# Kernel tuning notes

Measured on AMD Instinct MI355X. Metric: run time of the kernel, lower is better.

## Reference

```python
import jax, jax.numpy as jnp
import numpy as np

SEQ_LEN = 512
DIM = 256
HEADS = 8
DIM_HEAD = 32
INNER = HEADS * DIM_HEAD
BATCH = 1
LN_EPS = 1e-5


def setup_inputs() -> dict:
    key = jax.random.key(0)
    ks = jax.random.split(key, 6)
    # kaiming_uniform_(a=sqrt(5)) on [L, in, out] -> bound = 1/sqrt(fan_in) with fan_in = in_dim*out_dim? 
    # torch computes fan_in from dims [1:] => fan_in = in_dim (dim of -2) * ... in practice bound ~ sqrt(1/fan_in);
    # exact init distribution is irrelevant for correctness testing, use uniform(+-1/sqrt(DIM)).
    s = 1.0 / np.sqrt(DIM)
    so = 1.0 / np.sqrt(INNER)
    return {
        "x": jax.random.normal(ks[0], (BATCH, SEQ_LEN, DIM), jnp.float32),
        "Wq": jax.random.uniform(ks[1], (SEQ_LEN, DIM, INNER), jnp.float32, -s, s),
        "Wk": jax.random.uniform(ks[2], (SEQ_LEN, DIM, INNER), jnp.float32, -s, s),
        "Wv": jax.random.uniform(ks[3], (SEQ_LEN, DIM, INNER), jnp.float32, -s, s),
        "gamma": jnp.ones((DIM,), jnp.float32),
        "beta": jnp.zeros((DIM,), jnp.float32),
        "Wo": jax.random.uniform(ks[4], (INNER, DIM), jnp.float32, -so, so),
        "bo": jnp.zeros((DIM,), jnp.float32),
    }


def reference(x, Wq, Wk, Wv, gamma, beta, Wo, bo):
    b, n, dim = x.shape
    h, dh = HEADS, DIM_HEAD
    # LayerNorm
    mu = jnp.mean(x, axis=-1, keepdims=True)
    var = jnp.mean((x - mu) ** 2, axis=-1, keepdims=True)
    xn = (x - mu) / jnp.sqrt(var + LN_EPS) * gamma + beta
    # Per-relative-index projections: pd[b, r, m, e] = xn[b, m] @ W[r]
    qd = jnp.einsum('bmc,rce->brme', xn, Wq)
    kd = jnp.einsum('bmc,rce->brme', xn, Wk)
    vd = jnp.einsum('bmc,rce->brme', xn, Wv)
    i = jnp.arange(n)
    # to_q / to_v index map: max(0, i - j); to_k (after rearrange swap) uses min(0, m - n) + n - 1
    rq = jnp.maximum(0, i[:, None] - i[None, :])          # [n(query), m(key)]
    rk = jnp.minimum(0, i[None, :] - i[:, None]) + n - 1  # [n, m]
    # q[b,n,m,e] = qd[b, rq[n,m], m]; k[b,n,m,e] = kd[b, rk[n,m], n]; v like q
    q_full = qd[:, rq, i[None, :], :].reshape(b, n, n, h, dh)
    k_full = kd[:, rk, i[:, None], :].reshape(b, n, n, h, dh)
    v_full = vd[:, rq, i[None, :], :].reshape(b, n, n, h, dh)
    scale = dh ** -0.5
    dots = jnp.einsum('bnmhd,bnmhd->bhnm', q_full, k_full) * scale
    causal = i[:, None] >= i[None, :]  # tril
    dots = jnp.where(causal[None, None], dots, -jnp.inf)
    attn = jax.nn.softmax(dots, axis=-1)
    out = jnp.einsum('bhnm,bnmhd->bnhd', attn, v_full).reshape(b, n, h * dh)
    return out @ Wo + bo
```

## Files before the change

### kernel.cpp

```cpp
#include <hip/hip_runtime.h>
#include <hip/hip_bf16.h>

typedef unsigned short u16;
typedef unsigned int   u32;
typedef __bf16 bf16x8 __attribute__((ext_vector_type(8)));
typedef float  f32x4  __attribute__((ext_vector_type(4)));
typedef u32    u32x4  __attribute__((ext_vector_type(4)));
typedef u32    u32x2  __attribute__((ext_vector_type(2)));

#define TRI_TOTAL 131328

__device__ __forceinline__ float b2f(u16 u) {
    return __builtin_bit_cast(float, ((u32)u) << 16);
}
__device__ __forceinline__ u16 f2b(float f) {
    u32 u = __builtin_bit_cast(u32, f);
    return (u16)((u + 0x7fffu + ((u >> 16) & 1u)) >> 16);
}
__device__ __forceinline__ int pcol(int col) {
    return (((col & 7) ^ ((col >> 3) & 7)) << 4);
}

__global__ void __launch_bounds__(256) ln_kernel(const float* __restrict__ x,
                                                 const float* __restrict__ g,
                                                 const float* __restrict__ b,
                                                 u16* __restrict__ xn) {
    int n = blockIdx.x, t = threadIdx.x;
    float v = x[n * 256 + t];
    __shared__ float red[4];
    float s = v;
    #pragma unroll
    for (int o = 32; o >= 1; o >>= 1) s += __shfl_xor(s, o);
    if ((t & 63) == 0) red[t >> 6] = s;
    __syncthreads();
    float mu = (red[0] + red[1] + red[2] + red[3]) * (1.0f / 256.0f);
    float d = v - mu;
    __syncthreads();
    float s2 = d * d;
    #pragma unroll
    for (int o = 32; o >= 1; o >>= 1) s2 += __shfl_xor(s2, o);
    if ((t & 63) == 0) red[t >> 6] = s2;
    __syncthreads();
    float var = (red[0] + red[1] + red[2] + red[3]) * (1.0f / 256.0f);
    float y = d * rsqrtf(var + 1e-5f) * g[t] + b[t];
    xn[n * 256 + t] = f2b(y);
}

__global__ void __launch_bounds__(256) proj_kernel(
        const u16* __restrict__ xn,
        const float* __restrict__ Wq, const float* __restrict__ Wk,
        const float* __restrict__ Wv,
        u16* __restrict__ Qa, u16* __restrict__ Ka, u16* __restrict__ Va) {
    __shared__ u16 Wl[64 * 256];
    __shared__ u16 Al[64 * 256];

    int bid = blockIdx.x;
    int which = bid >> 11;
    int rr = bid & 2047;
    int r  = (which == 1) ? (511 - (rr >> 2)) : (rr >> 2);
    int cs = rr & 3;
    const float* W = (which == 0) ? Wq : ((which == 1) ? Wk : Wv);
    u16* Out       = (which == 0) ? Qa : ((which == 1) ? Ka : Va);
    int rows  = (which == 1) ? (r + 1) : (512 - r);
    int pbase = (which == 1) ? (511 - r) : 0;
    int nbase = (which == 1) ? (511 - r) : r;

    int t = threadIdx.x;
    int c0 = cs * 64;

    int srow   = t >> 5;
    int slot16 = (t & 31) * 16;
    char* adp = (char*)Al + srow * 512 + (slot16 ^ (srow << 4));
    u32x4 ar0, ar1, ar2, ar3, ar4, ar5, ar6, ar7;

#define A_LOAD(M0) do {                                                       \
    int gg;                                                                   \
    gg = pbase + (M0) +  0 + srow; if (gg > 511) gg = 511;                    \
    ar0 = *(const u32x4*)((const char*)xn + (size_t)gg * 512 + slot16);       \
    gg = pbase + (M0) +  8 + srow; if (gg > 511) gg = 511;                    \
    ar1 = *(const u32x4*)((const char*)xn + (size_t)gg * 512 + slot16);       \
    gg = pbase + (M0) + 16 + srow; if (gg > 511) gg = 511;                    \
    ar2 = *(const u32x4*)((const char*)xn + (size_t)gg * 512 + slot16);       \
    gg = pbase + (M0) + 24 + srow; if (gg > 511) gg = 511;                    \
    ar3 = *(const u32x4*)((const char*)xn + (size_t)gg * 512 + slot16);       \
    gg = pbase + (M0) + 32 + srow; if (gg > 511) gg = 511;                    \
    ar4 = *(const u32x4*)((const char*)xn + (size_t)gg * 512 + slot16);       \
    gg = pbase + (M0) + 40 + srow; if (gg > 511) gg = 511;                    \
    ar5 = *(const u32x4*)((const char*)xn + (size_t)gg * 512 + slot16);       \
    gg = pbase + (M0) + 48 + srow; if (gg > 511) gg = 511;                    \
    ar6 = *(const u32x4*)((const char*)xn + (size_t)gg * 512 + slot16);       \
    gg = pbase + (M0) + 56 + srow; if (gg > 511) gg = 511;                    \
    ar7 = *(const u32x4*)((const char*)xn + (size_t)gg * 512 + slot16);       \
} while (0)

#define A_WRITE() do {                                                        \
    *(u32x4*)(adp + 0 * 4096) = ar0;                                          \
    *(u32x4*)(adp + 1 * 4096) = ar1;                                          \
    *(u32x4*)(adp + 2 * 4096) = ar2;                                          \
    *(u32x4*)(adp + 3 * 4096) = ar3;                                          \
    *(u32x4*)(adp + 4 * 4096) = ar4;                                          \
    *(u32x4*)(adp + 5 * 4096) = ar5;                                          \
    *(u32x4*)(adp + 6 * 4096) = ar6;                                          \
    *(u32x4*)(adp + 7 * 4096) = ar7;                                          \
} while (0)

    {
        int c4 = (t & 15) * 4;
        int kq = t >> 4;
        const float* wp = W + ((size_t)r << 16) + c0 + c4 + (size_t)(kq * 4) * 256;
        f32x4 w00 = *(const f32x4*)(wp + 0);
        f32x4 w01 = *(const f32x4*)(wp + 256);
        f32x4 w02 = *(const f32x4*)(wp + 512);
        f32x4 w03 = *(const f32x4*)(wp + 768);
        f32x4 w10 = *(const f32x4*)(wp + 16384 + 0);
        f32x4 w11 = *(const f32x4*)(wp + 16384 + 256);
        f32x4 w12 = *(const f32x4*)(wp + 16384 + 512);
        f32x4 w13 = *(const f32x4*)(wp + 16384 + 768);
        f32x4 w20 = *(const f32x4*)(wp + 32768 + 0);
        f32x4 w21 = *(const f32x4*)(wp + 32768 + 256);
        f32x4 w22 = *(const f32x4*)(wp + 32768 + 512);
        f32x4 w23 = *(const f32x4*)(wp + 32768 + 768);
        f32x4 w30 = *(const f32x4*)(wp + 49152 + 0);
        f32x4 w31 = *(const f32x4*)(wp + 49152 + 256);
        f32x4 w32 = *(const f32x4*)(wp + 49152 + 512);
        f32x4 w33 = *(const f32x4*)(wp + 49152 + 768);
        A_LOAD(0);
#define WLW(IT, VA, VB, VC, VD) {                                             \
        int kbase2 = (kq * 4 + (IT) * 64) * 2;                                \
        _Pragma("unroll")                                                     \
        for (int i = 0; i < 4; ++i) {                                         \
            int col = c4 + i;                                                 \
            u32 lo = (u32)f2b(VA[i]) | ((u32)f2b(VB[i]) << 16);               \
            u32 hi = (u32)f2b(VC[i]) | ((u32)f2b(VD[i]) << 16);               \
            u32x2 pr; pr[0] = lo; pr[1] = hi;                                 \
            *(u32x2*)((char*)Wl + col * 512 + (kbase2 ^ pcol(col))) = pr;     \
        }                                                                     \
    }
        WLW(0, w00, w01, w02, w03)
        WLW(1, w10, w11, w12, w13)
        WLW(2, w20, w21, w22, w23)
        WLW(3, w30, w31, w32, w33)
#undef WLW
    }

    int wv  = t >> 6;
    int rg  = wv >> 1;
    int cg  = wv & 1;
    int L   = t & 63;
    int l15 = L & 15, l4 = L >> 4;
    const char* wb = (const char*)Wl;
    const char* a_base = (const char*)Al + (rg * 32 + l15) * 512;
    int am = (l15 & 7) << 4;
    int cA = cg * 32 + l15, cB = cA + 16;
    int swA = pcol(cA), swB = pcol(cB);

    for (int m0 = 0; m0 < rows; m0 += 64) {
        A_WRITE();
        __syncthreads();
        if (m0 + 64 < rows) A_LOAD(m0 + 64);

        f32x4 acc00 = {}, acc01 = {}, acc10 = {}, acc11 = {};
#define KS(ks) {                                                              \
        int kb = (ks) * 64 + l4 * 16;                                         \
        bf16x8 a0 = *(const bf16x8*)(a_base + (kb ^ am));                     \
        bf16x8 a1 = *(const bf16x8*)(a_base + 16 * 512 + (kb ^ am));          \
        bf16x8 b0 = *(const bf16x8*)(wb + cA * 512 + (kb ^ swA));             \
        bf16x8 b1 = *(const bf16x8*)(wb + cB * 512 + (kb ^ swB));             \
        acc00 = __builtin_amdgcn_mfma_f32_16x16x32_bf16(a0, b0, acc00, 0, 0, 0); \
        acc01 = __builtin_amdgcn_mfma_f32_16x16x32_bf16(a0, b1, acc01, 0, 0, 0); \
        acc10 = __builtin_amdgcn_mfma_f32_16x16x32_bf16(a1, b0, acc10, 0, 0, 0); \
        acc11 = __builtin_amdgcn_mfma_f32_16x16x32_bf16(a1, b1, acc11, 0, 0, 0); \
    }
        KS(0) KS(1) KS(2) KS(3) KS(4) KS(5) KS(6) KS(7)
#undef KS

        #pragma unroll
        for (int rf = 0; rf < 2; ++rf) {
            #pragma unroll
            for (int j = 0; j < 4; ++j) {
                int ml = m0 + rg * 32 + rf * 16 + l4 * 4 + j;
                if (ml < rows) {
                    int nout = nbase + ml;
                    size_t prow = (size_t)(nout * (nout + 1) / 2) + (size_t)ml;
                    u16* op = Out + prow * 256 + c0 + cg * 32 + l15;
                    f32x4 va = rf ? acc10 : acc00;
                    f32x4 vb = rf ? acc11 : acc01;
                    op[0]  = f2b(va[j]);
                    op[16] = f2b(vb[j]);
                }
            }
        }
        __syncthreads();
    }
#undef A_LOAD
#undef A_WRITE
}

__global__ void __launch_bounds__(256) attn_kernel(const u16* __restrict__ Qa,
                                                   const u16* __restrict__ Ka,
                                                   const u16* __restrict__ Va,
                                                   float* __restrict__ ao) {
    int n = blockIdx.x, t = threadIdx.x;
    __shared__ float pbuf[512 * 9];
    __shared__ float linv[8];
    int band = n + 1;
    size_t rb = (size_t)(n * (n + 1) / 2);

    int h = t & 7, mi = t >> 3;
    for (int m0 = 0; m0 < band; m0 += 32) {
        int m = m0 + mi;
        float d = -1e30f;
        if (m < band) {
            const char* qp = (const char*)Qa + (rb + m) * 512 + h * 64;
            const char* kp = (const char*)Ka + (rb + m) * 512 + h * 64;
            float acc = 0.f;
            #pragma unroll
            for (int cch = 0; cch < 4; ++cch) {
                u32x4 qv = *reinterpret_cast<const u32x4*>(qp + cch * 16);
                u32x4 kv = *reinterpret_cast<const u32x4*>(kp + cch * 16);
                #pragma unroll
                for (int i = 0; i < 4; ++i) {
                    float ql = __builtin_bit_cast(float, qv[i] << 16);
                    float qh = __builtin_bit_cast(float, qv[i] & 0xffff0000u);
                    float kl = __builtin_bit_cast(float, kv[i] << 16);
                    float kh = __builtin_bit_cast(float, kv[i] & 0xffff0000u);
                    acc += ql * kl + qh * kh;
                }
            }
            d = acc * 0.17677669529663687f;
        }
        pbuf[m * 9 + h] = d;
    }
    __syncthreads();

    int wv = t >> 6, L = t & 63;
    for (int s = 0; s < 2; ++s) {
        int hh = wv + s * 4;
        float mx = -1e30f;
        for (int m = L; m < band; m += 64) mx = fmaxf(mx, pbuf[m * 9 + hh]);
        #pragma unroll
        for (int o = 32; o >= 1; o >>= 1) mx = fmaxf(mx, __shfl_xor(mx, o));
        float sum = 0.f;
        for (int m = L; m < band; m += 64) {
            float p = __expf(pbuf[m * 9 + hh] - mx);
            pbuf[m * 9 + hh] = p;
            sum += p;
        }
        #pragma unroll
        for (int o = 32; o >= 1; o >>= 1) sum += __shfl_xor(sum, o);
        if (L == 0) linv[hh] = 1.0f / sum;
    }
    __syncthreads();

    int h2 = t >> 5;
    const char* vp = (const char*)Va + rb * 512 + (size_t)t * 2;
    const float* pb = pbuf + h2;
    float a0 = 0, a1 = 0, a2 = 0, a3 = 0;
    int m = 0;
    for (; m + 4 <= band; m += 4) {
        a0 += pb[(m + 0) * 9] * b2f(*(const u16*)(vp + (size_t)(m + 0) * 512));
        a1 += pb[(m + 1) * 9] * b2f(*(const u16*)(vp + (size_t)(m + 1) * 512));
        a2 += pb[(m + 2) * 9] * b2f(*(const u16*)(vp + (size_t)(m + 2) * 512));
        a3 += pb[(m + 3) * 9] * b2f(*(const u16*)(vp + (size_t)(m + 3) * 512));
    }
    for (; m < band; ++m)
        a0 += pb[m * 9] * b2f(*(const u16*)(vp + (size_t)m * 512));
    ao[n * 256 + t] = ((a0 + a1) + (a2 + a3)) * linv[h2];
}

__global__ void __launch_bounds__(256) outproj_kernel(const float* __restrict__ ao,
                                                      const float* __restrict__ Wo,
                                                      const float* __restrict__ bo,
                                                      float* __restrict__ out) {
    int n = blockIdx.x, e = threadIdx.x;
    const float* a = ao + n * 256;
    float c0 = bo[e], c1 = 0, c2 = 0, c3 = 0;
    for (int c = 0; c < 256; c += 4) {
        c0 += a[c + 0] * Wo[(c + 0) * 256 + e];
        c1 += a[c + 1] * Wo[(c + 1) * 256 + e];
        c2 += a[c + 2] * Wo[(c + 2) * 256 + e];
        c3 += a[c + 3] * Wo[(c + 3) * 256 + e];
    }
    out[n * 256 + e] = (c0 + c1) + (c2 + c3);
}

extern "C" void kernel_launch(void* const* d_in, const int* in_sizes, int n_in,
                              void* d_out, int out_size, void* d_ws, size_t ws_size,
                              hipStream_t stream) {
    const float* x     = (const float*)d_in[0];
    const float* Wq    = (const float*)d_in[1];
    const float* Wk    = (const float*)d_in[2];
    const float* Wv    = (const float*)d_in[3];
    const float* gamma = (const float*)d_in[4];
    const float* beta  = (const float*)d_in[5];
    const float* Wo    = (const float*)d_in[6];
    const float* bo    = (const float*)d_in[7];
    float* out = (float*)d_out;

    char* ws = (char*)d_ws;
    u16* xn = (u16*)ws;
    size_t off = (size_t)512 * 256 * 2;
    u16* Qa = (u16*)(ws + off); off += (size_t)TRI_TOTAL * 256 * 2;
    u16* Ka = (u16*)(ws + off); off += (size_t)TRI_TOTAL * 256 * 2;
    u16* Va = (u16*)(ws + off); off += (size_t)TRI_TOTAL * 256 * 2;
    float* ao = (float*)(ws + off);

    ln_kernel<<<512, 256, 0, stream>>>(x, gamma, beta, xn);
    proj_kernel<<<6144, 256, 0, stream>>>(xn, Wq, Wk, Wv, Qa, Ka, Va);
    attn_kernel<<<512, 256, 0, stream>>>(Qa, Ka, Va, ao);
    outproj_kernel<<<512, 256, 0, stream>>>(ao, Wo, bo, out);
}
```

Measured before the change: 275.1 us.

## Process two relative-index weight slices per projection block with prefetched second weights

```diff
diff --git a/kernel.cpp b/kernel.cpp
--- a/kernel.cpp
+++ b/kernel.cpp
@@ -46,7 +46,7 @@
     xn[n * 256 + t] = f2b(y);
 }
 
-__global__ void __launch_bounds__(256) proj_kernel(
+__global__ void __launch_bounds__(256, 2) proj_kernel(
         const u16* __restrict__ xn,
         const float* __restrict__ Wq, const float* __restrict__ Wk,
         const float* __restrict__ Wv,
@@ -55,15 +55,20 @@
     __shared__ u16 Al[64 * 256];
 
     int bid = blockIdx.x;
-    int which = bid >> 11;
-    int rr = bid & 2047;
-    int r  = (which == 1) ? (511 - (rr >> 2)) : (rr >> 2);
+    int which = bid >> 10;
+    int rr = bid & 1023;
+    int g  = rr >> 2;
     int cs = rr & 3;
     const float* W = (which == 0) ? Wq : ((which == 1) ? Wk : Wv);
     u16* Out       = (which == 0) ? Qa : ((which == 1) ? Ka : Va);
-    int rows  = (which == 1) ? (r + 1) : (512 - r);
-    int pbase = (which == 1) ? (511 - r) : 0;
-    int nbase = (which == 1) ? (511 - r) : r;
+    int rA = (which == 1) ? (511 - 2 * g) : (2 * g);
+    int rB = (which == 1) ? (510 - 2 * g) : (2 * g + 1);
+    int rows0 = (which == 1) ? (rA + 1) : (512 - rA);
+    int pb0   = (which == 1) ? (511 - rA) : 0;
+    int nb0   = (which == 1) ? (511 - rA) : rA;
+    int rows1 = (which == 1) ? (rB + 1) : (512 - rB);
+    int pb1   = (which == 1) ? (511 - rB) : 0;
+    int nb1   = (which == 1) ? (511 - rB) : rB;
 
     int t = threadIdx.x;
     int c0 = cs * 64;
@@ -73,23 +78,23 @@
     char* adp = (char*)Al + srow * 512 + (slot16 ^ (srow << 4));
     u32x4 ar0, ar1, ar2, ar3, ar4, ar5, ar6, ar7;
 
-#define A_LOAD(M0) do {                                                       \
+#define A_LOAD(PB, M0) do {                                                   \
     int gg;                                                                   \
-    gg = pbase + (M0) +  0 + srow; if (gg > 511) gg = 511;                    \
+    gg = (PB) + (M0) +  0 + srow; if (gg > 511) gg = 511;                     \
     ar0 = *(const u32x4*)((const char*)xn + (size_t)gg * 512 + slot16);       \
-    gg = pbase + (M0) +  8 + srow; if (gg > 511) gg = 511;                    \
+    gg = (PB) + (M0) +  8 + srow; if (gg > 511) gg = 511;                     \
     ar1 = *(const u32x4*)((const char*)xn + (size_t)gg * 512 + slot16);       \
-    gg = pbase + (M0) + 16 + srow; if (gg > 511) gg = 511;                    \
+    gg = (PB) + (M0) + 16 + srow; if (gg > 511) gg = 511;                     \
     ar2 = *(const u32x4*)((const char*)xn + (size_t)gg * 512 + slot16);       \
-    gg = pbase + (M0) + 24 + srow; if (gg > 511) gg = 511;                    \
+    gg = (PB) + (M0) + 24 + srow; if (gg > 511) gg = 511;                     \
     ar3 = *(const u32x4*)((const char*)xn + (size_t)gg * 512 + slot16);       \
-    gg = pbase + (M0) + 32 + srow; if (gg > 511) gg = 511;                    \
+    gg = (PB) + (M0) + 32 + srow; if (gg > 511) gg = 511;                     \
     ar4 = *(const u32x4*)((const char*)xn + (size_t)gg * 512 + slot16);       \
-    gg = pbase + (M0) + 40 + srow; if (gg > 511) gg = 511;                    \
+    gg = (PB) + (M0) + 40 + srow; if (gg > 511) gg = 511;                     \
     ar5 = *(const u32x4*)((const char*)xn + (size_t)gg * 512 + slot16);       \
-    gg = pbase + (M0) + 48 + srow; if (gg > 511) gg = 511;                    \
+    gg = (PB) + (M0) + 48 + srow; if (gg > 511) gg = 511;                     \
     ar6 = *(const u32x4*)((const char*)xn + (size_t)gg * 512 + slot16);       \
-    gg = pbase + (M0) + 56 + srow; if (gg > 511) gg = 511;                    \
+    gg = (PB) + (M0) + 56 + srow; if (gg > 511) gg = 511;                     \
     ar7 = *(const u32x4*)((const char*)xn + (size_t)gg * 512 + slot16);       \
 } while (0)
 
@@ -104,27 +109,27 @@
     *(u32x4*)(adp + 7 * 4096) = ar7;                                          \
 } while (0)
 
-    {
-        int c4 = (t & 15) * 4;
-        int kq = t >> 4;
-        const float* wp = W + ((size_t)r << 16) + c0 + c4 + (size_t)(kq * 4) * 256;
-        f32x4 w00 = *(const f32x4*)(wp + 0);
-        f32x4 w01 = *(const f32x4*)(wp + 256);
-        f32x4 w02 = *(const f32x4*)(wp + 512);
-        f32x4 w03 = *(const f32x4*)(wp + 768);
-        f32x4 w10 = *(const f32x4*)(wp + 16384 + 0);
-        f32x4 w11 = *(const f32x4*)(wp + 16384 + 256);
-        f32x4 w12 = *(const f32x4*)(wp + 16384 + 512);
-        f32x4 w13 = *(const f32x4*)(wp + 16384 + 768);
-        f32x4 w20 = *(const f32x4*)(wp + 32768 + 0);
-        f32x4 w21 = *(const f32x4*)(wp + 32768 + 256);
-        f32x4 w22 = *(const f32x4*)(wp + 32768 + 512);
-        f32x4 w23 = *(const f32x4*)(wp + 32768 + 768);
-        f32x4 w30 = *(const f32x4*)(wp + 49152 + 0);
-        f32x4 w31 = *(const f32x4*)(wp + 49152 + 256);
-        f32x4 w32 = *(const f32x4*)(wp + 49152 + 512);
-        f32x4 w33 = *(const f32x4*)(wp + 49152 + 768);
-        A_LOAD(0);
+    int c4 = (t & 15) * 4;
+    int kq = t >> 4;
+    f32x4 w00, w01, w02, w03, w10, w11, w12, w13;
+    f32x4 w20, w21, w22, w23, w30, w31, w32, w33;
+
+#define W_LOAD(R) do {                                                        \
+    const float* wp = W + ((size_t)(R) << 16) + c0 + c4 + (size_t)(kq * 4) * 256; \
+    w00 = *(const f32x4*)(wp + 0);           w01 = *(const f32x4*)(wp + 256); \
+    w02 = *(const f32x4*)(wp + 512);         w03 = *(const f32x4*)(wp + 768); \
+    w10 = *(const f32x4*)(wp + 16384 + 0);   w11 = *(const f32x4*)(wp + 16384 + 256); \
+    w12 = *(const f32x4*)(wp + 16384 + 512); w13 = *(const f32x4*)(wp + 16384 + 768); \
+    w20 = *(const f32x4*)(wp + 32768 + 0);   w21 = *(const f32x4*)(wp + 32768 + 256); \
+    w22 = *(const f32x4*)(wp + 32768 + 512); w23 = *(const f32x4*)(wp + 32768 + 768); \
+    w30 = *(const f32x4*)(wp + 49152 + 0);   w31 = *(const f32x4*)(wp + 49152 + 256); \
+    w32 = *(const f32x4*)(wp + 49152 + 512); w33 = *(const f32x4*)(wp + 49152 + 768); \
+} while (0)
+
+#define W_PIN() asm volatile("" :: "v"(w00), "v"(w01), "v"(w02), "v"(w03),    \
+    "v"(w10), "v"(w11), "v"(w12), "v"(w13), "v"(w20), "v"(w21), "v"(w22),     \
+    "v"(w23), "v"(w30), "v"(w31), "v"(w32), "v"(w33))
+
 #define WLW(IT, VA, VB, VC, VD) {                                             \
         int kbase2 = (kq * 4 + (IT) * 64) * 2;                                \
         _Pragma("unroll")                                                     \
@@ -136,12 +141,12 @@
             *(u32x2*)((char*)Wl + col * 512 + (kbase2 ^ pcol(col))) = pr;     \
         }                                                                     \
     }
-        WLW(0, w00, w01, w02, w03)
-        WLW(1, w10, w11, w12, w13)
-        WLW(2, w20, w21, w22, w23)
-        WLW(3, w30, w31, w32, w33)
-#undef WLW
-    }
+#define WL_WRITE() do {                                                       \
+        WLW(0, w00, w01, w02, w03)                                            \
+        WLW(1, w10, w11, w12, w13)                                            \
+        WLW(2, w20, w21, w22, w23)                                            \
+        WLW(3, w30, w31, w32, w33)                                            \
+} while (0)
 
     int wv  = t >> 6;
     int rg  = wv >> 1;
@@ -154,12 +159,6 @@
     int cA = cg * 32 + l15, cB = cA + 16;
     int swA = pcol(cA), swB = pcol(cB);
 
-    for (int m0 = 0; m0 < rows; m0 += 64) {
-        A_WRITE();
-        __syncthreads();
-        if (m0 + 64 < rows) A_LOAD(m0 + 64);
-
-        f32x4 acc00 = {}, acc01 = {}, acc10 = {}, acc11 = {};
 #define KS(ks) {                                                              \
         int kb = (ks) * 64 + l4 * 16;                                         \
         bf16x8 a0 = *(const bf16x8*)(a_base + (kb ^ am));                     \
@@ -171,29 +170,56 @@
         acc10 = __builtin_amdgcn_mfma_f32_16x16x32_bf16(a1, b0, acc10, 0, 0, 0); \
         acc11 = __builtin_amdgcn_mfma_f32_16x16x32_bf16(a1, b1, acc11, 0, 0, 0); \
     }
-        KS(0) KS(1) KS(2) KS(3) KS(4) KS(5) KS(6) KS(7)
+
+#define MTILE(M0, ROWS, NB, PREF) {                                           \
+        A_WRITE();                                                            \
+        __syncthreads();                                                      \
+        PREF                                                                  \
+        f32x4 acc00 = {}, acc01 = {}, acc10 = {}, acc11 = {};                 \
+        KS(0) KS(1) KS(2) KS(3) KS(4) KS(5) KS(6) KS(7)                       \
+        _Pragma("unroll")                                                     \
+        for (int rf = 0; rf < 2; ++rf) {                                      \
+            _Pragma("unroll")                                                 \
+            for (int j = 0; j < 4; ++j) {                                     \
+                int ml = (M0) + rg * 32 + rf * 16 + l4 * 4 + j;               \
+                if (ml < (ROWS)) {                                            \
+                    int nout = (NB) + ml;                                     \
+                    size_t prow = (size_t)(nout * (nout + 1) / 2) + (size_t)ml; \
+                    u16* op = Out + prow * 256 + c0 + cg * 32 + l15;          \
+                    f32x4 va = rf ? acc10 : acc00;                            \
+                    f32x4 vb = rf ? acc11 : acc01;                            \
+                    op[0]  = f2b(va[j]);                                      \
+                    op[16] = f2b(vb[j]);                                      \
+                }                                                             \
+            }                                                                 \
+        }                                                                     \
+        __syncthreads();                                                      \
+    }
+
+    W_LOAD(rA);
+    A_LOAD(pb0, 0);
+    WL_WRITE();
+    MTILE(0, rows0, nb0,
+          { W_LOAD(rB); W_PIN();
+            if (64 < rows0) { A_LOAD(pb0, 64); } else { A_LOAD(pb1, 0); } })
+    for (int m0 = 64; m0 < rows0; m0 += 64) {
+        MTILE(m0, rows0, nb0,
+              { if (m0 + 64 < rows0) { A_LOAD(pb0, m0 + 64); }
+                else { A_LOAD(pb1, 0); } })
+    }
+    WL_WRITE();
+    for (int m0 = 0; m0 < rows1; m0 += 64) {
+        MTILE(m0, rows1, nb1,
+              { if (m0 + 64 < rows1) { A_LOAD(pb1, m0 + 64); } })
+    }
+#undef MTILE
 #undef KS
-
-        #pragma unroll
-        for (int rf = 0; rf < 2; ++rf) {
-            #pragma unroll
-            for (int j = 0; j < 4; ++j) {
-                int ml = m0 + rg * 32 + rf * 16 + l4 * 4 + j;
-                if (ml < rows) {
-                    int nout = nbase + ml;
-                    size_t prow = (size_t)(nout * (nout + 1) / 2) + (size_t)ml;
-                    u16* op = Out + prow * 256 + c0 + cg * 32 + l15;
-                    f32x4 va = rf ? acc10 : acc00;
-                    f32x4 vb = rf ? acc11 : acc01;
-                    op[0]  = f2b(va[j]);
-                    op[16] = f2b(vb[j]);
-                }
-            }
-        }
-        __syncthreads();
-    }
+#undef WL_WRITE
+#undef WLW
+#undef W_PIN
+#undef W_LOAD
+#undef A_WRITE
 #undef A_LOAD
-#undef A_WRITE
 }
 
 __global__ void __launch_bounds__(256) attn_kernel(const u16* __restrict__ Qa,
@@ -306,7 +332,7 @@
     float* ao = (float*)(ws + off);
 
     ln_kernel<<<512, 256, 0, stream>>>(x, gamma, beta, xn);
-    proj_kernel<<<6144, 256, 0, stream>>>(xn, Wq, Wk, Wv, Qa, Ka, Va);
+    proj_kernel<<<3072, 256, 0, stream>>>(xn, Wq, Wk, Wv, Qa, Ka, Va);
     attn_kernel<<<512, 256, 0, stream>>>(Qa, Ka, Va, ao);
     outproj_kernel<<<512, 256, 0, stream>>>(ao, Wo, bo, out);
 }
```

New measurement: 276.4 us. About the same (+0.4%).

## Keep projection weight fragments in registers instead of shared memory

Applied to the files above, without the earlier changes.

```diff
diff --git a/kernel.cpp b/kernel.cpp
--- a/kernel.cpp
+++ b/kernel.cpp
@@ -6,7 +6,6 @@
 typedef __bf16 bf16x8 __attribute__((ext_vector_type(8)));
 typedef float  f32x4  __attribute__((ext_vector_type(4)));
 typedef u32    u32x4  __attribute__((ext_vector_type(4)));
-typedef u32    u32x2  __attribute__((ext_vector_type(2)));
 
 #define TRI_TOTAL 131328
 
@@ -16,9 +15,6 @@
 __device__ __forceinline__ u16 f2b(float f) {
     u32 u = __builtin_bit_cast(u32, f);
     return (u16)((u + 0x7fffu + ((u >> 16) & 1u)) >> 16);
-}
-__device__ __forceinline__ int pcol(int col) {
-    return (((col & 7) ^ ((col >> 3) & 7)) << 4);
 }
 
 __global__ void __launch_bounds__(256) ln_kernel(const float* __restrict__ x,
@@ -46,12 +42,11 @@
     xn[n * 256 + t] = f2b(y);
 }
 
-__global__ void __launch_bounds__(256) proj_kernel(
+__global__ void __launch_bounds__(256, 2) proj_kernel(
         const u16* __restrict__ xn,
         const float* __restrict__ Wq, const float* __restrict__ Wk,
         const float* __restrict__ Wv,
         u16* __restrict__ Qa, u16* __restrict__ Ka, u16* __restrict__ Va) {
-    __shared__ u16 Wl[64 * 256];
     __shared__ u16 Al[64 * 256];
 
     int bid = blockIdx.x;
@@ -67,6 +62,11 @@
 
     int t = threadIdx.x;
     int c0 = cs * 64;
+    int wv  = t >> 6;
+    int rg  = wv >> 1;
+    int cg  = wv & 1;
+    int L   = t & 63;
+    int l15 = L & 15, l4 = L >> 4;
 
     int srow   = t >> 5;
     int slot16 = (t & 31) * 16;
@@ -104,55 +104,27 @@
     *(u32x4*)(adp + 7 * 4096) = ar7;                                          \
 } while (0)
 
-    {
-        int c4 = (t & 15) * 4;
-        int kq = t >> 4;
-        const float* wp = W + ((size_t)r << 16) + c0 + c4 + (size_t)(kq * 4) * 256;
-        f32x4 w00 = *(const f32x4*)(wp + 0);
-        f32x4 w01 = *(const f32x4*)(wp + 256);
-        f32x4 w02 = *(const f32x4*)(wp + 512);
-        f32x4 w03 = *(const f32x4*)(wp + 768);
-        f32x4 w10 = *(const f32x4*)(wp + 16384 + 0);
-        f32x4 w11 = *(const f32x4*)(wp + 16384 + 256);
-        f32x4 w12 = *(const f32x4*)(wp + 16384 + 512);
-        f32x4 w13 = *(const f32x4*)(wp + 16384 + 768);
-        f32x4 w20 = *(const f32x4*)(wp + 32768 + 0);
-        f32x4 w21 = *(const f32x4*)(wp + 32768 + 256);
-        f32x4 w22 = *(const f32x4*)(wp + 32768 + 512);
-        f32x4 w23 = *(const f32x4*)(wp + 32768 + 768);
-        f32x4 w30 = *(const f32x4*)(wp + 49152 + 0);
-        f32x4 w31 = *(const f32x4*)(wp + 49152 + 256);
-        f32x4 w32 = *(const f32x4*)(wp + 49152 + 512);
-        f32x4 w33 = *(const f32x4*)(wp + 49152 + 768);
-        A_LOAD(0);
-#define WLW(IT, VA, VB, VC, VD) {                                             \
-        int kbase2 = (kq * 4 + (IT) * 64) * 2;                                \
-        _Pragma("unroll")                                                     \
-        for (int i = 0; i < 4; ++i) {                                         \
-            int col = c4 + i;                                                 \
-            u32 lo = (u32)f2b(VA[i]) | ((u32)f2b(VB[i]) << 16);               \
-            u32 hi = (u32)f2b(VC[i]) | ((u32)f2b(VD[i]) << 16);               \
-            u32x2 pr; pr[0] = lo; pr[1] = hi;                                 \
-            *(u32x2*)((char*)Wl + col * 512 + (kbase2 ^ pcol(col))) = pr;     \
-        }                                                                     \
-    }
-        WLW(0, w00, w01, w02, w03)
-        WLW(1, w10, w11, w12, w13)
-        WLW(2, w20, w21, w22, w23)
-        WLW(3, w30, w31, w32, w33)
-#undef WLW
-    }
-
-    int wv  = t >> 6;
-    int rg  = wv >> 1;
-    int cg  = wv & 1;
-    int L   = t & 63;
-    int l15 = L & 15, l4 = L >> 4;
-    const char* wb = (const char*)Wl;
+    A_LOAD(0);
+
+    const float* wbase = W + ((size_t)r << 16) + c0 + cg * 32 + l15;
+    bf16x8 b00, b01, b02, b03, b04, b05, b06, b07;
+    bf16x8 b10, b11, b12, b13, b14, b15, b16, b17;
+#define BLOAD(HF, KSI, DST) {                                                 \
+    const float* wp = wbase + (size_t)((KSI) * 32 + l4 * 8) * 256 + (HF) * 16;\
+    u32x4 pk;                                                                 \
+    pk[0] = (u32)f2b(wp[0])    | ((u32)f2b(wp[256])  << 16);                  \
+    pk[1] = (u32)f2b(wp[512])  | ((u32)f2b(wp[768])  << 16);                  \
+    pk[2] = (u32)f2b(wp[1024]) | ((u32)f2b(wp[1280]) << 16);                  \
+    pk[3] = (u32)f2b(wp[1536]) | ((u32)f2b(wp[1792]) << 16);                  \
+    DST = __builtin_bit_cast(bf16x8, pk); }
+    BLOAD(0, 0, b00) BLOAD(0, 1, b01) BLOAD(0, 2, b02) BLOAD(0, 3, b03)
+    BLOAD(0, 4, b04) BLOAD(0, 5, b05) BLOAD(0, 6, b06) BLOAD(0, 7, b07)
+    BLOAD(1, 0, b10) BLOAD(1, 1, b11) BLOAD(1, 2, b12) BLOAD(1, 3, b13)
+    BLOAD(1, 4, b14) BLOAD(1, 5, b15) BLOAD(1, 6, b16) BLOAD(1, 7, b17)
+#undef BLOAD
+
     const char* a_base = (const char*)Al + (rg * 32 + l15) * 512;
     int am = (l15 & 7) << 4;
-    int cA = cg * 32 + l15, cB = cA + 16;
-    int swA = pcol(cA), swB = pcol(cB);
 
     for (int m0 = 0; m0 < rows; m0 += 64) {
         A_WRITE();
@@ -164,12 +136,10 @@
         int kb = (ks) * 64 + l4 * 16;                                         \
         bf16x8 a0 = *(const bf16x8*)(a_base + (kb ^ am));                     \
         bf16x8 a1 = *(const bf16x8*)(a_base + 16 * 512 + (kb ^ am));          \
-        bf16x8 b0 = *(const bf16x8*)(wb + cA * 512 + (kb ^ swA));             \
-        bf16x8 b1 = *(const bf16x8*)(wb + cB * 512 + (kb ^ swB));             \
-        acc00 = __builtin_amdgcn_mfma_f32_16x16x32_bf16(a0, b0, acc00, 0, 0, 0); \
-        acc01 = __builtin_amdgcn_mfma_f32_16x16x32_bf16(a0, b1, acc01, 0, 0, 0); \
-        acc10 = __builtin_amdgcn_mfma_f32_16x16x32_bf16(a1, b0, acc10, 0, 0, 0); \
-        acc11 = __builtin_amdgcn_mfma_f32_16x16x32_bf16(a1, b1, acc11, 0, 0, 0); \
+        acc00 = __builtin_amdgcn_mfma_f32_16x16x32_bf16(a0, b0##ks, acc00, 0, 0, 0); \
+        acc01 = __builtin_amdgcn_mfma_f32_16x16x32_bf16(a0, b1##ks, acc01, 0, 0, 0); \
+        acc10 = __builtin_amdgcn_mfma_f32_16x16x32_bf16(a1, b0##ks, acc10, 0, 0, 0); \
+        acc11 = __builtin_amdgcn_mfma_f32_16x16x32_bf16(a1, b1##ks, acc11, 0, 0, 0); \
     }
         KS(0) KS(1) KS(2) KS(3) KS(4) KS(5) KS(6) KS(7)
 #undef KS
@@ -192,8 +162,8 @@
         }
         __syncthreads();
     }
+#undef A_WRITE
 #undef A_LOAD
-#undef A_WRITE
 }
 
 __global__ void __launch_bounds__(256) attn_kernel(const u16* __restrict__ Qa,
```

Measured after the change: 312.7 us. 1.14x slower.

## Double-buffer projection A tiles via direct global-to-LDS loads, keep W in registers

Applied to the files above, without the earlier changes.

```diff
diff --git a/kernel.cpp b/kernel.cpp
--- a/kernel.cpp
+++ b/kernel.cpp
@@ -19,6 +19,11 @@
 }
 __device__ __forceinline__ int pcol(int col) {
     return (((col & 7) ^ ((col >> 3) & 7)) << 4);
+}
+__device__ __forceinline__ void gload_lds16(const void* g, void* l) {
+    __builtin_amdgcn_global_load_lds(
+        (const __attribute__((address_space(1))) void*)g,
+        (__attribute__((address_space(3))) void*)l, 16, 0, 0);
 }
 
 __global__ void __launch_bounds__(256) ln_kernel(const float* __restrict__ x,
@@ -51,8 +56,9 @@
         const float* __restrict__ Wq, const float* __restrict__ Wk,
         const float* __restrict__ Wv,
         u16* __restrict__ Qa, u16* __restrict__ Ka, u16* __restrict__ Va) {
-    __shared__ u16 Wl[64 * 256];
-    __shared__ u16 Al[64 * 256];
+    __shared__ char lds[65536];
+    char* buf0 = lds;
+    char* buf1 = lds + 32768;
 
     int bid = blockIdx.x;
     int which = bid >> 11;
@@ -67,42 +73,25 @@
 
     int t = threadIdx.x;
     int c0 = cs * 64;
-
-    int srow   = t >> 5;
-    int slot16 = (t & 31) * 16;
-    char* adp = (char*)Al + srow * 512 + (slot16 ^ (srow << 4));
-    u32x4 ar0, ar1, ar2, ar3, ar4, ar5, ar6, ar7;
-
-#define A_LOAD(M0) do {                                                       \
-    int gg;                                                                   \
-    gg = pbase + (M0) +  0 + srow; if (gg > 511) gg = 511;                    \
-    ar0 = *(const u32x4*)((const char*)xn + (size_t)gg * 512 + slot16);       \
-    gg = pbase + (M0) +  8 + srow; if (gg > 511) gg = 511;                    \
-    ar1 = *(const u32x4*)((const char*)xn + (size_t)gg * 512 + slot16);       \
-    gg = pbase + (M0) + 16 + srow; if (gg > 511) gg = 511;                    \
-    ar2 = *(const u32x4*)((const char*)xn + (size_t)gg * 512 + slot16);       \
-    gg = pbase + (M0) + 24 + srow; if (gg > 511) gg = 511;                    \
-    ar3 = *(const u32x4*)((const char*)xn + (size_t)gg * 512 + slot16);       \
-    gg = pbase + (M0) + 32 + srow; if (gg > 511) gg = 511;                    \
-    ar4 = *(const u32x4*)((const char*)xn + (size_t)gg * 512 + slot16);       \
-    gg = pbase + (M0) + 40 + srow; if (gg > 511) gg = 511;                    \
-    ar5 = *(const u32x4*)((const char*)xn + (size_t)gg * 512 + slot16);       \
-    gg = pbase + (M0) + 48 + srow; if (gg > 511) gg = 511;                    \
-    ar6 = *(const u32x4*)((const char*)xn + (size_t)gg * 512 + slot16);       \
-    gg = pbase + (M0) + 56 + srow; if (gg > 511) gg = 511;                    \
-    ar7 = *(const u32x4*)((const char*)xn + (size_t)gg * 512 + slot16);       \
+    int wv  = t >> 6;
+    int rg  = wv >> 1;
+    int cg  = wv & 1;
+    int L   = t & 63;
+    int l15 = L & 15, l4 = L >> 4;
+
+#define DMA_TILE(DST, M0) do {                                                \
+    _Pragma("unroll")                                                         \
+    for (int j = 0; j < 8; ++j) {                                             \
+        int lrow = wv * 16 + 2 * j + (L >> 5);                                \
+        int grow = pbase + (M0) + lrow; if (grow > 511) grow = 511;           \
+        const char* gp = (const char*)xn + (size_t)grow * 512                 \
+                         + (((L & 31) ^ (lrow & 7)) << 4);                    \
+        char* lp = (DST) + (wv * 16 + 2 * j) * 512;                           \
+        gload_lds16(gp, lp);                                                  \
+    }                                                                         \
 } while (0)
 
-#define A_WRITE() do {                                                        \
-    *(u32x4*)(adp + 0 * 4096) = ar0;                                          \
-    *(u32x4*)(adp + 1 * 4096) = ar1;                                          \
-    *(u32x4*)(adp + 2 * 4096) = ar2;                                          \
-    *(u32x4*)(adp + 3 * 4096) = ar3;                                          \
-    *(u32x4*)(adp + 4 * 4096) = ar4;                                          \
-    *(u32x4*)(adp + 5 * 4096) = ar5;                                          \
-    *(u32x4*)(adp + 6 * 4096) = ar6;                                          \
-    *(u32x4*)(adp + 7 * 4096) = ar7;                                          \
-} while (0)
+    DMA_TILE(buf1, 0);
 
     {
         int c4 = (t & 15) * 4;
@@ -124,7 +113,6 @@
         f32x4 w31 = *(const f32x4*)(wp + 49152 + 256);
         f32x4 w32 = *(const f32x4*)(wp + 49152 + 512);
         f32x4 w33 = *(const f32x4*)(wp + 49152 + 768);
-        A_LOAD(0);
 #define WLW(IT, VA, VB, VC, VD) {                                             \
         int kbase2 = (kq * 4 + (IT) * 64) * 2;                                \
         _Pragma("unroll")                                                     \
@@ -133,7 +121,7 @@
             u32 lo = (u32)f2b(VA[i]) | ((u32)f2b(VB[i]) << 16);               \
             u32 hi = (u32)f2b(VC[i]) | ((u32)f2b(VD[i]) << 16);               \
             u32x2 pr; pr[0] = lo; pr[1] = hi;                                 \
-            *(u32x2*)((char*)Wl + col * 512 + (kbase2 ^ pcol(col))) = pr;     \
+            *(u32x2*)(buf0 + col * 512 + (kbase2 ^ pcol(col))) = pr;          \
         }                                                                     \
     }
         WLW(0, w00, w01, w02, w03)
@@ -142,34 +130,40 @@
         WLW(3, w30, w31, w32, w33)
 #undef WLW
     }
-
-    int wv  = t >> 6;
-    int rg  = wv >> 1;
-    int cg  = wv & 1;
-    int L   = t & 63;
-    int l15 = L & 15, l4 = L >> 4;
-    const char* wb = (const char*)Wl;
-    const char* a_base = (const char*)Al + (rg * 32 + l15) * 512;
+    __syncthreads();
+
+    bf16x8 b00, b01, b02, b03, b04, b05, b06, b07;
+    bf16x8 b10, b11, b12, b13, b14, b15, b16, b17;
+#define BEXT(HF, KSI, DST) {                                                  \
+    int col = cg * 32 + (HF) * 16 + l15;                                      \
+    int kb = (KSI) * 64 + l4 * 16;                                            \
+    DST = *(const bf16x8*)(buf0 + col * 512 + (kb ^ pcol(col))); }
+    BEXT(0, 0, b00) BEXT(0, 1, b01) BEXT(0, 2, b02) BEXT(0, 3, b03)
+    BEXT(0, 4, b04) BEXT(0, 5, b05) BEXT(0, 6, b06) BEXT(0, 7, b07)
+    BEXT(1, 0, b10) BEXT(1, 1, b11) BEXT(1, 2, b12) BEXT(1, 3, b13)
+    BEXT(1, 4, b14) BEXT(1, 5, b15) BEXT(1, 6, b16) BEXT(1, 7, b17)
+#undef BEXT
+    __syncthreads();
+
     int am = (l15 & 7) << 4;
-    int cA = cg * 32 + l15, cB = cA + 16;
-    int swA = pcol(cA), swB = pcol(cB);
-
-    for (int m0 = 0; m0 < rows; m0 += 64) {
-        A_WRITE();
-        __syncthreads();
-        if (m0 + 64 < rows) A_LOAD(m0 + 64);
-
+    int nt = (rows + 63) >> 6;
+    char* cur = buf1;
+    char* alt = buf0;
+
+    for (int i = 0; i < nt; ++i) {
+        int m0 = i << 6;
+        if (i + 1 < nt) DMA_TILE(alt, m0 + 64);
+
+        const char* abase = cur + (rg * 32 + l15) * 512;
         f32x4 acc00 = {}, acc01 = {}, acc10 = {}, acc11 = {};
 #define KS(ks) {                                                              \
         int kb = (ks) * 64 + l4 * 16;                                         \
-        bf16x8 a0 = *(const bf16x8*)(a_base + (kb ^ am));                     \
-        bf16x8 a1 = *(const bf16x8*)(a_base + 16 * 512 + (kb ^ am));          \
-        bf16x8 b0 = *(const bf16x8*)(wb + cA * 512 + (kb ^ swA));             \
-        bf16x8 b1 = *(const bf16x8*)(wb + cB * 512 + (kb ^ swB));             \
-        acc00 = __builtin_amdgcn_mfma_f32_16x16x32_bf16(a0, b0, acc00, 0, 0, 0); \
-        acc01 = __builtin_amdgcn_mfma_f32_16x16x32_bf16(a0, b1, acc01, 0, 0, 0); \
-        acc10 = __builtin_amdgcn_mfma_f32_16x16x32_bf16(a1, b0, acc10, 0, 0, 0); \
-        acc11 = __builtin_amdgcn_mfma_f32_16x16x32_bf16(a1, b1, acc11, 0, 0, 0); \
+        bf16x8 a0 = *(const bf16x8*)(abase + (kb ^ am));                      \
+        bf16x8 a1 = *(const bf16x8*)(abase + 16 * 512 + (kb ^ am));           \
+        acc00 = __builtin_amdgcn_mfma_f32_16x16x32_bf16(a0, b0##ks, acc00, 0, 0, 0); \
+        acc01 = __builtin_amdgcn_mfma_f32_16x16x32_bf16(a0, b1##ks, acc01, 0, 0, 0); \
+        acc10 = __builtin_amdgcn_mfma_f32_16x16x32_bf16(a1, b0##ks, acc10, 0, 0, 0); \
+        acc11 = __builtin_amdgcn_mfma_f32_16x16x32_bf16(a1, b1##ks, acc11, 0, 0, 0); \
     }
         KS(0) KS(1) KS(2) KS(3) KS(4) KS(5) KS(6) KS(7)
 #undef KS
@@ -191,9 +185,9 @@
             }
         }
         __syncthreads();
-    }
-#undef A_LOAD
-#undef A_WRITE
+        char* tmp = cur; cur = alt; alt = tmp;
+    }
+#undef DMA_TILE
 }
 
 __global__ void __launch_bounds__(256) attn_kernel(const u16* __restrict__ Qa,
```

Measured after the change: 268.0 us. 1.03x faster.
